# Optimization experiments

Hardware: AMD Instinct MI355X
Metric: run time of the kernel (lower is better)

The kernel has to match this reference:

```python
import jax, jax.numpy as jnp
import numpy as np

N_NODES = 50000
N_EDGES = 800000
IN_CH, HID_CH, OUT_CH = 128, 128, 64


def _gcn_conv(x, W, b, src, dst, n):
    """PyG GCNConv: self-loops + symmetric norm + linear + scatter-add + bias."""
    loop = jnp.arange(n, dtype=src.dtype)
    src_sl = jnp.concatenate([src, loop])  # [E+N]
    dst_sl = jnp.concatenate([dst, loop])
    # degree computed on edges incl. self-loops (edge weight 1)
    deg = jax.ops.segment_sum(jnp.ones_like(dst_sl, dtype=x.dtype), dst_sl,
                              num_segments=n)
    dinv = jnp.where(deg > 0, jax.lax.rsqrt(deg), 0.0)
    norm = dinv[src_sl] * dinv[dst_sl]  # [E+N]
    xw = x @ W  # [N, F_out]
    msg = xw[src_sl] * norm[:, None]  # gather + scale, [E+N, F_out]
    out = jax.ops.segment_sum(msg, dst_sl, num_segments=n)
    return out + b


def setup_inputs() -> dict:
    key = jax.random.key(0)
    ks = jax.random.split(key, 5)
    x = jax.random.normal(ks[0], (N_NODES, IN_CH), dtype=jnp.float32)
    edge_index = jax.random.randint(ks[1], (2, N_EDGES), 0, N_NODES, dtype=jnp.int64)
    s1 = 1.0 / np.sqrt(IN_CH)
    s2 = 1.0 / np.sqrt(HID_CH)
    W1 = jax.random.normal(ks[2], (IN_CH, HID_CH), dtype=jnp.float32) * s1
    W2 = jax.random.normal(ks[3], (HID_CH, HID_CH), dtype=jnp.float32) * s2
    W3 = jax.random.normal(ks[4], (HID_CH, OUT_CH), dtype=jnp.float32) * s2
    return {
        "x": x, "edge_index": edge_index,
        "W1": W1, "b1": jnp.zeros((HID_CH,), jnp.float32),
        "W2": W2, "b2": jnp.zeros((HID_CH,), jnp.float32),
        "W3": W3, "b3": jnp.zeros((OUT_CH,), jnp.float32),
    }


def reference(x, edge_index, W1, b1, W2, b2, W3, b3):
    n = x.shape[0]
    src, dst = edge_index[0], edge_index[1]
    # dropout(p=0.6) is identity in eval mode
    h = jax.nn.relu(_gcn_conv(x, W1, b1, src, dst, n))
    h = jax.nn.relu(_gcn_conv(h, W2, b2, src, dst, n))
    out = _gcn_conv(h, W3, b3, src, dst, n)
    return out
```

## Files before the change

kernel.cpp:

```cpp
#include <hip/hip_runtime.h>
#include <cstdint>

#define CAP 32768
#define CHUNK 2048

typedef __attribute__((ext_vector_type(8))) short bf8_t;
typedef __attribute__((ext_vector_type(4))) float f4_t;

__device__ __forceinline__ uint32_t f_to_bf(float f) {
    union { float f; uint32_t u; } v; v.f = f;
    uint32_t u = v.u;
    return (u + 0x7fffu + ((u >> 16) & 1u)) >> 16;
}
__device__ __forceinline__ float bf_to_f(uint32_t h) {
    union { uint32_t u; float f; } v; v.u = h << 16; return v.f;
}
__device__ __forceinline__ float2 bf2_to_f2(uint32_t u) {
    union { uint32_t u; float f; } a, b;
    a.u = u << 16; b.u = u & 0xffff0000u;
    float2 r; r.x = a.f; r.y = b.f; return r;
}
__device__ __forceinline__ void fma8(float* acc, uint4 u, float d) {
    float2 p0 = bf2_to_f2(u.x), p1 = bf2_to_f2(u.y);
    float2 p2 = bf2_to_f2(u.z), p3 = bf2_to_f2(u.w);
    acc[0] += p0.x * d; acc[1] += p0.y * d;
    acc[2] += p1.x * d; acc[3] += p1.y * d;
    acc[4] += p2.x * d; acc[5] += p2.y * d;
    acc[6] += p3.x * d; acc[7] += p3.y * d;
}

__device__ __forceinline__ int detect64(const int* __restrict__ e32) {
    return (e32[1] | e32[3] | e32[5] | e32[7]) == 0;
}
__device__ __forceinline__ int edge_at(const void* edges, int is64, int idx) {
    if (is64) return (int)((const long long*)edges)[idx];
    return ((const int*)edges)[idx];
}

__global__ __launch_bounds__(256) void prep_kernel(
    const float* __restrict__ W1, const float* __restrict__ W2,
    const float* __restrict__ W3,
    uint16_t* w1h, uint16_t* w1l, uint16_t* w2h, uint16_t* w2l,
    uint16_t* w3h, uint16_t* w3l, int* __restrict__ bucket_cur,
    int* __restrict__ done) {
    if (blockIdx.x == 160) {
        if (threadIdx.x < 64) bucket_cur[threadIdx.x] = threadIdx.x * CAP;
        if (threadIdx.x == 64) *done = 0;
        return;
    }
    int idx = blockIdx.x * 256 + threadIdx.x;
    const float* W; uint16_t* oh; uint16_t* ol; int FOUT; int e;
    if (idx < 16384)      { W = W1; oh = w1h; ol = w1l; FOUT = 128; e = idx; }
    else if (idx < 32768) { W = W2; oh = w2h; ol = w2l; FOUT = 128; e = idx - 16384; }
    else                  { W = W3; oh = w3h; ol = w3l; FOUT = 64;  e = idx - 32768; }
    int j = e & 7;
    int lane = (e >> 3) & 63;
    int rem = e >> 9;
    int NT = FOUT >> 4;
    int nt = rem % NT, kc = rem / NT;
    int k = kc * 32 + ((lane >> 4) << 3) + j;
    int c = nt * 16 + (lane & 15);
    float v = W[(size_t)k * FOUT + c];
    uint32_t h = f_to_bf(v);
    uint32_t l = f_to_bf(v - bf_to_f(h));
    oh[e] = (uint16_t)h;
    ol[e] = (uint16_t)l;
}

__device__ __forceinline__ void gemm1_body(
    const float* __restrict__ A, const uint16_t* __restrict__ Wfhi,
    const uint16_t* __restrict__ Wflo, uint16_t* __restrict__ Yout,
    int n, int cp, int tile0, int tstride, int lane) {
    constexpr int NT = 8, NTW = 2;
    int ntiles = (n + 15) >> 4;
    bf8_t wh[NTW][4], wl[NTW][4];
#pragma unroll
    for (int t = 0; t < NTW; t++) {
        int nt = cp * NTW + t;
#pragma unroll
        for (int kc = 0; kc < 4; kc++) {
            size_t b = ((size_t)(kc * NT + nt) * 64 + lane) * 8;
            wh[t][kc] = *(const bf8_t*)&Wfhi[b];
            wl[t][kc] = *(const bf8_t*)&Wflo[b];
        }
    }
    int row_in = lane & 15;
    int koff = (lane >> 4) << 3;
    int colb = lane & 15;
    int rq = (lane >> 4) << 2;
    for (int tile = tile0; tile < ntiles; tile += tstride) {
        int R = tile << 4;
        int arow = R + row_in; if (arow >= n) arow = n - 1;
        const float* ap = A + (size_t)arow * 128 + koff;
        bf8_t ah[4], al[4];
#pragma unroll
        for (int kc = 0; kc < 4; kc++) {
            float4 pv = *(const float4*)(ap + kc * 32);
            float4 qv = *(const float4*)(ap + kc * 32 + 4);
            float vv[8] = {pv.x, pv.y, pv.z, pv.w, qv.x, qv.y, qv.z, qv.w};
#pragma unroll
            for (int j = 0; j < 8; j++) {
                uint32_t h = f_to_bf(vv[j]);
                ah[kc][j] = (short)h;
                al[kc][j] = (short)f_to_bf(vv[j] - bf_to_f(h));
            }
        }
        f4_t acc[NTW];
#pragma unroll
        for (int t = 0; t < NTW; t++) acc[t] = (f4_t){0.f, 0.f, 0.f, 0.f};
#pragma unroll
        for (int kc = 0; kc < 4; kc++) {
#pragma unroll
            for (int t = 0; t < NTW; t++) {
                acc[t] = __builtin_amdgcn_mfma_f32_16x16x32_bf16(ah[kc], wh[t][kc], acc[t], 0, 0, 0);
                acc[t] = __builtin_amdgcn_mfma_f32_16x16x32_bf16(ah[kc], wl[t][kc], acc[t], 0, 0, 0);
                acc[t] = __builtin_amdgcn_mfma_f32_16x16x32_bf16(al[kc], wh[t][kc], acc[t], 0, 0, 0);
            }
        }
#pragma unroll
        for (int t = 0; t < NTW; t++) {
            int c = (cp * NTW + t) * 16 + colb;
#pragma unroll
            for (int r = 0; r < 4; r++) {
                int row = R + rq + r;
                if (row < n)
                    Yout[(size_t)row * 128 + c] = (uint16_t)f_to_bf(acc[t][r]);
            }
        }
    }
}

__global__ __launch_bounds__(256) void scatter_gemm1_kernel(
    const void* __restrict__ ei, int* __restrict__ bucket_cur,
    int2* __restrict__ buckets, int E, int sbcnt,
    const float* __restrict__ x, const uint16_t* __restrict__ w1h,
    const uint16_t* __restrict__ w1l, uint16_t* __restrict__ y1, int n) {
    int tid = threadIdx.x;
    if ((int)blockIdx.x < sbcnt) {
        __shared__ int cnt[64];
        int base = blockIdx.x * CHUNK;
        int is64 = detect64((const int*)ei);
        if (tid < 64) cnt[tid] = 0;
        __syncthreads();
        int dloc[8];
#pragma unroll
        for (int it = 0; it < 8; it++) {
            int i = base + it * 256 + tid;
            int d = (i < E) ? edge_at(ei, is64, E + i) : -1;
            dloc[it] = d;
            if (d >= 0) atomicAdd(&cnt[d >> 10], 1);
        }
        __syncthreads();
        if (tid < 64) {
            int v = cnt[tid];
            cnt[tid] = atomicAdd(&bucket_cur[tid], v);
        }
        __syncthreads();
#pragma unroll
        for (int it = 0; it < 8; it++) {
            int i = base + it * 256 + tid;
            if (dloc[it] >= 0) {
                int s = edge_at(ei, is64, i);
                int p = atomicAdd(&cnt[dloc[it] >> 10], 1);
                buckets[p] = make_int2(s, dloc[it]);
            }
        }
    } else {
        int lane = tid & 63, wid = tid >> 6;
        gemm1_body(x, w1h, w1l, y1, n, wid, blockIdx.x - sbcnt,
                   gridDim.x - sbcnt, lane);
    }
}

__global__ __launch_bounds__(512) void csr_build_kernel(
    const int2* __restrict__ buckets, const int* __restrict__ bucket_cur,
    int* __restrict__ row_ptr, int* __restrict__ bsum, float* __restrict__ dinv,
    int* __restrict__ col, uint16_t* __restrict__ y1, int* __restrict__ done,
    int n, int nbuck) {
    __shared__ int cnt[1024];
    __shared__ int sb[1024];
    __shared__ float divals[1024];
    __shared__ int s_bo;
    int b = blockIdx.x, tid = threadIdx.x;
    int base = b << 10;
    int lim = min(1024, n - base);
    if (lim <= 0) return;
    int ecnt = bucket_cur[b] - b * CAP;
    const int2* ebase = buckets + (size_t)b * CAP;
    for (int i = tid; i < 1024; i += 512) cnt[i] = 0;
    __syncthreads();
    for (int i = tid; i < ecnt; i += 512)
        atomicAdd(&cnt[ebase[i].y - base], 1);
    __syncthreads();
    for (int i = tid; i < lim; i += 512) {
        float di = rsqrtf((float)(cnt[i] + 1));
        divals[i] = di;
        dinv[base + i] = di;
    }
    __syncthreads();
    int* a = cnt; int* s = sb;
    for (int st = 1; st < 1024; st <<= 1) {
        for (int i = tid; i < 1024; i += 512)
            s[i] = a[i] + ((i >= st) ? a[i - st] : 0);
        __syncthreads();
        int* t = a; a = s; s = t;
    }
    if (tid == 0) {
        bsum[b] = a[1023];
        __threadfence();
        atomicAdd(done, 1);
    }
    {
        uint32_t* y1w = (uint32_t*)y1 + ((size_t)base << 6);
        int total = lim << 6;
        for (int idx = tid; idx < total; idx += 512) {
            float di = divals[idx >> 6];
            uint32_t u = y1w[idx];
            float2 v = bf2_to_f2(u);
            y1w[idx] = f_to_bf(v.x * di) | (f_to_bf(v.y * di) << 16);
        }
    }
    if (tid == 0) {
        while (atomicAdd(done, 0) < nbuck) __builtin_amdgcn_s_sleep(8);
    }
    __syncthreads();
    __threadfence();
    if (tid < 64) {
        int lane = tid;
        int v = (lane < nbuck) ? bsum[lane] : 0;
        int incl = v;
#pragma unroll
        for (int off = 1; off < 64; off <<= 1) {
            int t = __shfl_up(incl, off);
            if (lane >= off) incl += t;
        }
        int tot = __shfl(incl, nbuck - 1);
        int bo = (b > 0) ? __shfl(incl, b - 1) : 0;
        if (lane == 0) {
            s_bo = bo;
            if (b == nbuck - 1) row_ptr[n] = tot;
        }
    }
    __syncthreads();
    int bo = s_bo;
    int* cur = s;
    for (int i = tid; i < lim; i += 512) {
        int v = ((i > 0) ? a[i - 1] : 0) + bo;
        row_ptr[base + i] = v;
        cur[i] = v;
    }
    __syncthreads();
    for (int i = tid; i < ecnt; i += 512) {
        int2 e = ebase[i];
        int p = atomicAdd(&cur[e.y - base], 1);
        col[p] = e.x;
    }
}

template <int FOUT>
__global__ __launch_bounds__(256) void agg_gemm_kernel(
    const uint16_t* __restrict__ Yin, const int* __restrict__ row_ptr,
    const int* __restrict__ col, const float* __restrict__ dinv,
    const float* __restrict__ bias,
    const uint16_t* __restrict__ Wfhi, const uint16_t* __restrict__ Wflo,
    uint16_t* __restrict__ Yout, int n) {
    __shared__ uint4 hs4[16 * 17];
    __shared__ uint4 ls4[16 * 17];
    int tid = threadIdx.x, wid = tid >> 6, lane = tid & 63;
    int base = blockIdx.x * 16;
    int g = lane & 15, j = lane >> 4;
    const uint4* Y4 = (const uint4*)Yin;

    float4 bb0 = *(const float4*)&bias[g * 8];
    float4 bb1 = *(const float4*)&bias[g * 8 + 4];
    float bb[8] = {bb0.x, bb0.y, bb0.z, bb0.w, bb1.x, bb1.y, bb1.z, bb1.w};

    for (int q = 0; q < 4; q++) {
        int r = wid * 4 + q, node = base + r;
        uint4 ph = (uint4){0, 0, 0, 0}, pl = (uint4){0, 0, 0, 0};
        if (node < n) {
            float di = dinv[node];
            float aA[8] = {}, aB[8] = {};
            {
                uint4 su = Y4[(size_t)node * 16 + g];
                fma8(aA, su, (j == 0) ? 1.f : 0.f);
            }
            int start = row_ptr[node], end = row_ptr[node + 1];
            for (int b = start; b < end; b += 64) {
                int cnt = min(64, end - b);
                int sv = (b + lane < end) ? col[b + lane] : 0;
                for (int k = 0; k < cnt; k += 8) {
                    int iA = k + j, iB = k + 4 + j;
                    int sA = __shfl(sv, iA & 63);
                    int sB = __shfl(sv, iB & 63);
                    float dA = (iA < cnt) ? 1.f : 0.f;
                    float dB = (iB < cnt) ? 1.f : 0.f;
                    uint4 uA = Y4[(size_t)sA * 16 + g];
                    uint4 uB = Y4[(size_t)sB * 16 + g];
                    fma8(aA, uA, dA);
                    fma8(aB, uB, dB);
                }
            }
            float o[8];
#pragma unroll
            for (int t = 0; t < 8; t++) o[t] = aA[t] + aB[t];
#pragma unroll
            for (int t = 0; t < 8; t++) o[t] += __shfl_xor(o[t], 16);
#pragma unroll
            for (int t = 0; t < 8; t++) o[t] += __shfl_xor(o[t], 32);
            uint32_t hh[8];
#pragma unroll
            for (int t = 0; t < 8; t++) {
                o[t] = fmaxf(o[t] * di + bb[t], 0.f);
                hh[t] = f_to_bf(o[t]);
            }
            ph = (uint4){hh[0] | (hh[1] << 16), hh[2] | (hh[3] << 16),
                         hh[4] | (hh[5] << 16), hh[6] | (hh[7] << 16)};
            uint32_t ll[8];
#pragma unroll
            for (int t = 0; t < 8; t++) ll[t] = f_to_bf(o[t] - bf_to_f(hh[t]));
            pl = (uint4){ll[0] | (ll[1] << 16), ll[2] | (ll[3] << 16),
                         ll[4] | (ll[5] << 16), ll[6] | (ll[7] << 16)};
        }
        if (j == 0) {
            hs4[r * 17 + g] = ph;
            ls4[r * 17 + g] = pl;
        }
    }
    __syncthreads();

    const uint16_t* hs = (const uint16_t*)hs4;
    const uint16_t* ls = (const uint16_t*)ls4;
    constexpr int NT = FOUT / 16;
    constexpr int NTW = NT / 4;
    constexpr int LDW = 136;
    int cp = wid;
    bf8_t wh[NTW][4], wl[NTW][4];
#pragma unroll
    for (int t = 0; t < NTW; t++) {
        int nt = cp * NTW + t;
#pragma unroll
        for (int kc = 0; kc < 4; kc++) {
            size_t b = ((size_t)(kc * NT + nt) * 64 + lane) * 8;
            wh[t][kc] = *(const bf8_t*)&Wfhi[b];
            wl[t][kc] = *(const bf8_t*)&Wflo[b];
        }
    }
    int koff = (lane >> 4) << 3;
    int colb = lane & 15;
    int rq = (lane >> 4) << 2;
    bf8_t ah[4], al[4];
#pragma unroll
    for (int kc = 0; kc < 4; kc++) {
        ah[kc] = *(const bf8_t*)(hs + (lane & 15) * LDW + koff + kc * 32);
        al[kc] = *(const bf8_t*)(ls + (lane & 15) * LDW + koff + kc * 32);
    }
    f4_t acc[NTW];
#pragma unroll
    for (int t = 0; t < NTW; t++) acc[t] = (f4_t){0.f, 0.f, 0.f, 0.f};
#pragma unroll
    for (int kc = 0; kc < 4; kc++) {
#pragma unroll
        for (int t = 0; t < NTW; t++) {
            acc[t] = __builtin_amdgcn_mfma_f32_16x16x32_bf16(ah[kc], wh[t][kc], acc[t], 0, 0, 0);
            acc[t] = __builtin_amdgcn_mfma_f32_16x16x32_bf16(ah[kc], wl[t][kc], acc[t], 0, 0, 0);
            acc[t] = __builtin_amdgcn_mfma_f32_16x16x32_bf16(al[kc], wh[t][kc], acc[t], 0, 0, 0);
        }
    }
#pragma unroll
    for (int t = 0; t < NTW; t++) {
        int c = (cp * NTW + t) * 16 + colb;
#pragma unroll
        for (int r = 0; r < 4; r++) {
            int row = base + rq + r;
            if (row < n) {
                float v = acc[t][r] * dinv[row];
                Yout[(size_t)row * FOUT + c] = (uint16_t)f_to_bf(v);
            }
        }
    }
}

__global__ __launch_bounds__(256) void agg_final_kernel(
    const uint16_t* __restrict__ Y, const int* __restrict__ row_ptr,
    const int* __restrict__ col, const float* __restrict__ dinv,
    const float* __restrict__ bias, float* __restrict__ out, int n) {
    int w = blockIdx.x * 4 + (threadIdx.x >> 6);
    int lane = threadIdx.x & 63;
    if (w >= n) return;
    int g = lane & 7, j = lane >> 3;
    const uint4* Y4 = (const uint4*)Y;
    float4 bb0 = *(const float4*)&bias[g * 8];
    float4 bb1 = *(const float4*)&bias[g * 8 + 4];
    float bb[8] = {bb0.x, bb0.y, bb0.z, bb0.w, bb1.x, bb1.y, bb1.z, bb1.w};

    float aA[8] = {}, aB[8] = {};
    {
        uint4 su = Y4[(size_t)w * 8 + g];
        fma8(aA, su, (j == 0) ? 1.f : 0.f);
    }
    int start = row_ptr[w], end = row_ptr[w + 1];
    for (int b = start; b < end; b += 64) {
        int cnt = min(64, end - b);
        int sv = (b + lane < end) ? col[b + lane] : 0;
        for (int k = 0; k < cnt; k += 16) {
            int iA = k + j, iB = k + 8 + j;
            int sA = __shfl(sv, iA & 63);
            int sB = __shfl(sv, iB & 63);
            float dA = (iA < cnt) ? 1.f : 0.f;
            float dB = (iB < cnt) ? 1.f : 0.f;
            uint4 uA = Y4[(size_t)sA * 8 + g];
            uint4 uB = Y4[(size_t)sB * 8 + g];
            fma8(aA, uA, dA);
            fma8(aB, uB, dB);
        }
    }
    float o[8];
#pragma unroll
    for (int t = 0; t < 8; t++) o[t] = aA[t] + aB[t];
#pragma unroll
    for (int t = 0; t < 8; t++) o[t] += __shfl_xor(o[t], 8);
#pragma unroll
    for (int t = 0; t < 8; t++) o[t] += __shfl_xor(o[t], 16);
#pragma unroll
    for (int t = 0; t < 8; t++) o[t] += __shfl_xor(o[t], 32);
    float di = dinv[w];
#pragma unroll
    for (int t = 0; t < 8; t++) o[t] = o[t] * di + bb[t];
    if (j == 0) {
        float4 o0 = {o[0], o[1], o[2], o[3]};
        float4 o1 = {o[4], o[5], o[6], o[7]};
        *(float4*)&out[(size_t)w * 64 + g * 8] = o0;
        *(float4*)&out[(size_t)w * 64 + g * 8 + 4] = o1;
    }
}

extern "C" void kernel_launch(void* const* d_in, const int* in_sizes, int n_in,
                              void* d_out, int out_size, void* d_ws, size_t ws_size,
                              hipStream_t stream) {
    const float* x  = (const float*)d_in[0];
    const void*  ei = d_in[1];
    const float* W1 = (const float*)d_in[2];
    const float* b1 = (const float*)d_in[3];
    const float* W2 = (const float*)d_in[4];
    const float* b2 = (const float*)d_in[5];
    const float* W3 = (const float*)d_in[6];
    const float* b3 = (const float*)d_in[7];
    int n = in_sizes[0] / 128;
    int E = in_sizes[1] / 2;
    int nbuck = (n + 1023) >> 10;

    char* p = (char*)d_ws;
    auto carve = [&](size_t bytes) {
        char* r = p;
        p += (bytes + 255) & ~(size_t)255;
        return r;
    };
    float*    dinv       = (float*)carve((size_t)n * 4);
    int*      row_ptr    = (int*)carve((size_t)(n + 1) * 4);
    int*      bsum       = (int*)carve(64 * 4);
    int*      bucket_cur = (int*)carve(64 * 4);
    int*      done       = (int*)carve(256);
    int*      col        = (int*)carve((size_t)E * 4);
    int2*     buckets    = (int2*)carve((size_t)64 * CAP * 8);
    uint16_t* y1         = (uint16_t*)carve((size_t)n * 128 * 2);
    uint16_t* y2         = (uint16_t*)carve((size_t)n * 128 * 2);
    uint16_t* y3         = (uint16_t*)carve((size_t)n * 64 * 2);
    uint16_t* w1h        = (uint16_t*)carve(128 * 128 * 2);
    uint16_t* w1l        = (uint16_t*)carve(128 * 128 * 2);
    uint16_t* w2h        = (uint16_t*)carve(128 * 128 * 2);
    uint16_t* w2l        = (uint16_t*)carve(128 * 128 * 2);
    uint16_t* w3h        = (uint16_t*)carve(128 * 64 * 2);
    uint16_t* w3l        = (uint16_t*)carve(128 * 64 * 2);

    int sbcnt = (E + CHUNK - 1) / CHUNK;
    int fb = (n + 15) / 16;

    prep_kernel<<<161, 256, 0, stream>>>(W1, W2, W3, w1h, w1l, w2h, w2l,
                                         w3h, w3l, bucket_cur, done);
    scatter_gemm1_kernel<<<sbcnt + 782, 256, 0, stream>>>(
        ei, bucket_cur, buckets, E, sbcnt, x, w1h, w1l, y1, n);
    csr_build_kernel<<<nbuck, 512, 0, stream>>>(
        buckets, bucket_cur, row_ptr, bsum, dinv, col, y1, done, n, nbuck);
    agg_gemm_kernel<128><<<fb, 256, 0, stream>>>(
        y1, row_ptr, col, dinv, b1, w2h, w2l, y2, n);
    agg_gemm_kernel<64><<<fb, 256, 0, stream>>>(
        y2, row_ptr, col, dinv, b2, w3h, w3l, y3, n);
    agg_final_kernel<<<(n + 3) / 4, 256, 0, stream>>>(
        y3, row_ptr, col, dinv, b3, (float*)d_out, n);
}
```

Measured before the change: 275.5 us.

## Use 256-node buckets for CSR build and apply source scaling in first aggregation

Shrinks destination buckets from 1024 to 256 nodes, which raises the CSR-build grid from about 49 to about 196 blocks so more CUs take part, and replaces the single-wave bucket prefix with a chunked scan that handles more than 64 buckets. The y1 rescale by dinv is removed from the CSR build kernel; the first aggregation instead multiplies each gathered source row by dinv[src]. This shortens the serial work in the spin-synchronised CSR kernel, at the cost of an extra dinv gather per edge in the first aggregation and a tighter per-bucket capacity of 8192 edges. The overflow margin relies on the edges being spread evenly across destinations.

```diff
diff --git a/kernel.cpp b/kernel.cpp
--- a/kernel.cpp
+++ b/kernel.cpp
@@ -1,7 +1,7 @@
 #include <hip/hip_runtime.h>
 #include <cstdint>
 
-#define CAP 32768
+#define CAP 8192
 #define CHUNK 2048
 
 typedef __attribute__((ext_vector_type(8))) short bf8_t;
@@ -44,8 +44,8 @@
     uint16_t* w3h, uint16_t* w3l, int* __restrict__ bucket_cur,
     int* __restrict__ done) {
     if (blockIdx.x == 160) {
-        if (threadIdx.x < 64) bucket_cur[threadIdx.x] = threadIdx.x * CAP;
-        if (threadIdx.x == 64) *done = 0;
+        bucket_cur[threadIdx.x] = threadIdx.x * CAP;
+        if (threadIdx.x == 0) *done = 0;
         return;
     }
     int idx = blockIdx.x * 256 + threadIdx.x;
@@ -137,10 +137,10 @@
     const uint16_t* __restrict__ w1l, uint16_t* __restrict__ y1, int n) {
     int tid = threadIdx.x;
     if ((int)blockIdx.x < sbcnt) {
-        __shared__ int cnt[64];
+        __shared__ int cnt[256];
         int base = blockIdx.x * CHUNK;
         int is64 = detect64((const int*)ei);
-        if (tid < 64) cnt[tid] = 0;
+        cnt[tid] = 0;
         __syncthreads();
         int dloc[8];
 #pragma unroll
@@ -148,12 +148,12 @@
             int i = base + it * 256 + tid;
             int d = (i < E) ? edge_at(ei, is64, E + i) : -1;
             dloc[it] = d;
-            if (d >= 0) atomicAdd(&cnt[d >> 10], 1);
+            if (d >= 0) atomicAdd(&cnt[d >> 8], 1);
         }
         __syncthreads();
-        if (tid < 64) {
+        {
             int v = cnt[tid];
-            cnt[tid] = atomicAdd(&bucket_cur[tid], v);
+            cnt[tid] = v ? atomicAdd(&bucket_cur[tid], v) : 0;
         }
         __syncthreads();
 #pragma unroll
@@ -161,7 +161,7 @@
             int i = base + it * 256 + tid;
             if (dloc[it] >= 0) {
                 int s = edge_at(ei, is64, i);
-                int p = atomicAdd(&cnt[dloc[it] >> 10], 1);
+                int p = atomicAdd(&cnt[dloc[it] >> 8], 1);
                 buckets[p] = make_int2(s, dloc[it]);
             }
         }
@@ -175,50 +175,35 @@
 __global__ __launch_bounds__(512) void csr_build_kernel(
     const int2* __restrict__ buckets, const int* __restrict__ bucket_cur,
     int* __restrict__ row_ptr, int* __restrict__ bsum, float* __restrict__ dinv,
-    int* __restrict__ col, uint16_t* __restrict__ y1, int* __restrict__ done,
-    int n, int nbuck) {
-    __shared__ int cnt[1024];
-    __shared__ int sb[1024];
-    __shared__ float divals[1024];
+    int* __restrict__ col, int* __restrict__ done, int n, int nbuck) {
+    __shared__ int cnt[256];
+    __shared__ int sb[256];
     __shared__ int s_bo;
     int b = blockIdx.x, tid = threadIdx.x;
-    int base = b << 10;
-    int lim = min(1024, n - base);
-    if (lim <= 0) return;
+    int base = b << 8;
+    int lim = min(256, n - base);
+    if (lim <= 0) {
+        if (tid == 0) { bsum[b] = 0; __threadfence(); atomicAdd(done, 1); }
+        return;
+    }
     int ecnt = bucket_cur[b] - b * CAP;
     const int2* ebase = buckets + (size_t)b * CAP;
-    for (int i = tid; i < 1024; i += 512) cnt[i] = 0;
+    if (tid < 256) cnt[tid] = 0;
     __syncthreads();
     for (int i = tid; i < ecnt; i += 512)
         atomicAdd(&cnt[ebase[i].y - base], 1);
     __syncthreads();
-    for (int i = tid; i < lim; i += 512) {
-        float di = rsqrtf((float)(cnt[i] + 1));
-        divals[i] = di;
-        dinv[base + i] = di;
-    }
-    __syncthreads();
+    if (tid < lim) dinv[base + tid] = rsqrtf((float)(cnt[tid] + 1));
     int* a = cnt; int* s = sb;
-    for (int st = 1; st < 1024; st <<= 1) {
-        for (int i = tid; i < 1024; i += 512)
-            s[i] = a[i] + ((i >= st) ? a[i - st] : 0);
+    for (int st = 1; st < 256; st <<= 1) {
+        if (tid < 256) s[tid] = a[tid] + ((tid >= st) ? a[tid - st] : 0);
         __syncthreads();
         int* t = a; a = s; s = t;
     }
     if (tid == 0) {
-        bsum[b] = a[1023];
+        bsum[b] = a[255];
         __threadfence();
         atomicAdd(done, 1);
-    }
-    {
-        uint32_t* y1w = (uint32_t*)y1 + ((size_t)base << 6);
-        int total = lim << 6;
-        for (int idx = tid; idx < total; idx += 512) {
-            float di = divals[idx >> 6];
-            uint32_t u = y1w[idx];
-            float2 v = bf2_to_f2(u);
-            y1w[idx] = f_to_bf(v.x * di) | (f_to_bf(v.y * di) << 16);
-        }
     }
     if (tid == 0) {
         while (atomicAdd(done, 0) < nbuck) __builtin_amdgcn_s_sleep(8);
@@ -227,27 +212,28 @@
     __threadfence();
     if (tid < 64) {
         int lane = tid;
-        int v = (lane < nbuck) ? bsum[lane] : 0;
-        int incl = v;
-#pragma unroll
-        for (int off = 1; off < 64; off <<= 1) {
-            int t = __shfl_up(incl, off);
-            if (lane >= off) incl += t;
-        }
-        int tot = __shfl(incl, nbuck - 1);
-        int bo = (b > 0) ? __shfl(incl, b - 1) : 0;
-        if (lane == 0) {
-            s_bo = bo;
-            if (b == nbuck - 1) row_ptr[n] = tot;
-        }
+        int carry = 0;
+        for (int c = 0; c < nbuck; c += 64) {
+            int idx = c + lane;
+            int v = (idx < nbuck) ? bsum[idx] : 0;
+            int incl = v;
+#pragma unroll
+            for (int off = 1; off < 64; off <<= 1) {
+                int t = __shfl_up(incl, off);
+                if (lane >= off) incl += t;
+            }
+            if (idx == b) s_bo = carry + (incl - v);
+            carry += __shfl(incl, 63);
+        }
+        if (lane == 0 && b == nbuck - 1) row_ptr[n] = carry;
     }
     __syncthreads();
     int bo = s_bo;
     int* cur = s;
-    for (int i = tid; i < lim; i += 512) {
-        int v = ((i > 0) ? a[i - 1] : 0) + bo;
-        row_ptr[base + i] = v;
-        cur[i] = v;
+    if (tid < lim) {
+        int v = ((tid > 0) ? a[tid - 1] : 0) + bo;
+        row_ptr[base + tid] = v;
+        cur[tid] = v;
     }
     __syncthreads();
     for (int i = tid; i < ecnt; i += 512) {
@@ -257,7 +243,7 @@
     }
 }
 
-template <int FOUT>
+template <int FOUT, bool SRC_SCALE>
 __global__ __launch_bounds__(256) void agg_gemm_kernel(
     const uint16_t* __restrict__ Yin, const int* __restrict__ row_ptr,
     const int* __restrict__ col, const float* __restrict__ dinv,
@@ -282,8 +268,9 @@
             float di = dinv[node];
             float aA[8] = {}, aB[8] = {};
             {
+                float sd = (j == 0) ? (SRC_SCALE ? di : 1.f) : 0.f;
                 uint4 su = Y4[(size_t)node * 16 + g];
-                fma8(aA, su, (j == 0) ? 1.f : 0.f);
+                fma8(aA, su, sd);
             }
             int start = row_ptr[node], end = row_ptr[node + 1];
             for (int b = start; b < end; b += 64) {
@@ -293,8 +280,8 @@
                     int iA = k + j, iB = k + 4 + j;
                     int sA = __shfl(sv, iA & 63);
                     int sB = __shfl(sv, iB & 63);
-                    float dA = (iA < cnt) ? 1.f : 0.f;
-                    float dB = (iB < cnt) ? 1.f : 0.f;
+                    float dA = (iA < cnt) ? (SRC_SCALE ? dinv[sA] : 1.f) : 0.f;
+                    float dB = (iB < cnt) ? (SRC_SCALE ? dinv[sB] : 1.f) : 0.f;
                     uint4 uA = Y4[(size_t)sA * 16 + g];
                     uint4 uB = Y4[(size_t)sB * 16 + g];
                     fma8(aA, uA, dA);
@@ -448,7 +435,7 @@
     const float* b3 = (const float*)d_in[7];
     int n = in_sizes[0] / 128;
     int E = in_sizes[1] / 2;
-    int nbuck = (n + 1023) >> 10;
+    int nbuck = (n + 255) >> 8;
 
     char* p = (char*)d_ws;
     auto carve = [&](size_t bytes) {
@@ -458,11 +445,11 @@
     };
     float*    dinv       = (float*)carve((size_t)n * 4);
     int*      row_ptr    = (int*)carve((size_t)(n + 1) * 4);
-    int*      bsum       = (int*)carve(64 * 4);
-    int*      bucket_cur = (int*)carve(64 * 4);
+    int*      bsum       = (int*)carve(256 * 4);
+    int*      bucket_cur = (int*)carve(256 * 4);
     int*      done       = (int*)carve(256);
     int*      col        = (int*)carve((size_t)E * 4);
-    int2*     buckets    = (int2*)carve((size_t)64 * CAP * 8);
+    int2*     buckets    = (int2*)carve((size_t)256 * CAP * 8);
     uint16_t* y1         = (uint16_t*)carve((size_t)n * 128 * 2);
     uint16_t* y2         = (uint16_t*)carve((size_t)n * 128 * 2);
     uint16_t* y3         = (uint16_t*)carve((size_t)n * 64 * 2);
@@ -478,13 +465,13 @@
 
     prep_kernel<<<161, 256, 0, stream>>>(W1, W2, W3, w1h, w1l, w2h, w2l,
                                          w3h, w3l, bucket_cur, done);
-    scatter_gemm1_kernel<<<sbcnt + 782, 256, 0, stream>>>(
+    scatter_gemm1_kernel<<<sbcnt + fb, 256, 0, stream>>>(
         ei, bucket_cur, buckets, E, sbcnt, x, w1h, w1l, y1, n);
     csr_build_kernel<<<nbuck, 512, 0, stream>>>(
-        buckets, bucket_cur, row_ptr, bsum, dinv, col, y1, done, n, nbuck);
-    agg_gemm_kernel<128><<<fb, 256, 0, stream>>>(
+        buckets, bucket_cur, row_ptr, bsum, dinv, col, done, n, nbuck);
+    agg_gemm_kernel<128, true><<<fb, 256, 0, stream>>>(
         y1, row_ptr, col, dinv, b1, w2h, w2l, y2, n);
-    agg_gemm_kernel<64><<<fb, 256, 0, stream>>>(
+    agg_gemm_kernel<64, false><<<fb, 256, 0, stream>>>(
         y2, row_ptr, col, dinv, b2, w3h, w3l, y3, n);
     agg_final_kernel<<<(n + 3) / 4, 256, 0, stream>>>(
         y3, row_ptr, col, dinv, b3, (float*)d_out, n);
```

Result: faster. 260.6 us (-5.4%).
